# Optimization experiments

Hardware: AMD Instinct MI355X
Metric: run time of the kernel (lower is better)

The kernel has to match this reference:

```python
import jax, jax.numpy as jnp
import numpy as np

B, T, C = 2, 2048, 1024
H = 16
HD = C // H  # 64
SCALE = 0.1 / (HD ** 0.5)


def setup_inputs() -> dict:
    key = jax.random.key(0)
    k1, k2, k3 = jax.random.split(key, 3)
    x = jax.random.normal(k1, (B, T, C), dtype=jnp.float32)
    W_attn = jax.random.normal(k2, (C, 3 * C), dtype=jnp.float32) * (C ** -0.5)
    b_attn = jnp.zeros((3 * C,), dtype=jnp.float32)
    W_proj = jax.random.normal(k3, (C, C), dtype=jnp.float32) * (C ** -0.5)
    b_proj = jnp.zeros((C,), dtype=jnp.float32)
    return {"x": x, "W_attn": W_attn, "b_attn": b_attn, "W_proj": W_proj, "b_proj": b_proj}


def reference(x, W_attn, b_attn, W_proj, b_proj):
    Bx, Tx, Cx = x.shape
    qkv = x @ W_attn + b_attn  # [B,T,3C]
    q, k, v = jnp.split(qkv, 3, axis=-1)
    # [B,T,C] -> [B,H,T,HD]
    q = q.reshape(Bx, Tx, H, HD).transpose(0, 2, 1, 3)
    k = k.reshape(Bx, Tx, H, HD).transpose(0, 2, 1, 3)
    v = v.reshape(Bx, Tx, H, HD).transpose(0, 2, 1, 3)
    # note the extra 0.1 factor baked into this module's scaling
    attn = jnp.einsum('bhqd,bhkd->bhqk', q, k) * SCALE
    causal = jnp.tril(jnp.ones((Tx, Tx), dtype=bool))
    attn = jnp.where(causal[None, None, :, :], attn, -jnp.inf)
    attn = jax.nn.softmax(attn, axis=-1)
    y = jnp.einsum('bhqk,bhkd->bhqd', attn, v)
    y = y.transpose(0, 2, 1, 3).reshape(Bx, Tx, Cx)
    return y @ W_proj + b_proj
```

## Files before the change

kernel.cpp:

```cpp
#include <hip/hip_runtime.h>

typedef unsigned short u16;
typedef unsigned int u32;
typedef float f32x4 __attribute__((ext_vector_type(4)));
typedef float f32x16 __attribute__((ext_vector_type(16)));
typedef __bf16 bf16x8 __attribute__((ext_vector_type(8)));
typedef u16 u16x8 __attribute__((ext_vector_type(8)));
typedef u32 u32x4 __attribute__((ext_vector_type(4)));

#define ATT_SCALE 0.0125f
#define LOG2E 1.4426950408889634f

__device__ __forceinline__ u16 f2bf(float x) {
  unsigned u = __builtin_bit_cast(unsigned, x);
  u += 0x7fffu + ((u >> 16) & 1u);
  return (u16)(u >> 16);
}

__device__ __forceinline__ u32 pack_bf16(float lo, float hi) {
  __bf16 a = (__bf16)lo, b = (__bf16)hi;
  return ((u32)__builtin_bit_cast(u16, b) << 16) | __builtin_bit_cast(u16, a);
}

__device__ __forceinline__ float fexp2(float x) {
  return __builtin_amdgcn_exp2f(x);
}

__device__ __forceinline__ f32x4 mfma16(u16x8 a, u16x8 b, f32x4 c) {
  return __builtin_amdgcn_mfma_f32_16x16x32_bf16(
      __builtin_bit_cast(bf16x8, a), __builtin_bit_cast(bf16x8, b), c, 0, 0, 0);
}

__device__ __forceinline__ f32x16 mfma32(u16x8 a, u16x8 b, f32x16 c) {
  return __builtin_amdgcn_mfma_f32_32x32x16_bf16(
      __builtin_bit_cast(bf16x8, a), __builtin_bit_cast(bf16x8, b), c, 0, 0, 0);
}

__device__ __forceinline__ void gl_lds16(const void* g, void* l) {
  __builtin_amdgcn_global_load_lds(
      (__attribute__((address_space(1))) void*)g,
      (__attribute__((address_space(3))) void*)l, 16, 0, 0);
}

__global__ void k_convert(const float* __restrict__ in, u16* __restrict__ out, int n) {
  int stride = gridDim.x * blockDim.x * 4;
  for (int i = (blockIdx.x * blockDim.x + threadIdx.x) * 4; i < n; i += stride) {
    float4 v = *(const float4*)&in[i];
    ushort4 o;
    o.x = f2bf(v.x); o.y = f2bf(v.y); o.z = f2bf(v.z); o.w = f2bf(v.w);
    *(ushort4*)&out[i] = o;
  }
}

__global__ void k_transpose(const float* __restrict__ in, u16* __restrict__ out,
                            int rows, int cols) {
  __shared__ float tile[32][33];
  int n0 = blockIdx.x * 32;
  int k0 = blockIdx.y * 32;
  int tx = threadIdx.x, ty = threadIdx.y;
#pragma unroll
  for (int i = 0; i < 32; i += 8)
    tile[ty + i][tx] = in[(size_t)(k0 + ty + i) * cols + n0 + tx];
  __syncthreads();
#pragma unroll
  for (int i = 0; i < 32; i += 8)
    out[(size_t)(n0 + ty + i) * rows + k0 + tx] = f2bf(tile[tx][ty + i]);
}

__global__ void k_gemm_qkv(const u16* __restrict__ A, const u16* __restrict__ Bt,
                           const float* __restrict__ bias,
                           u16* __restrict__ qb, u16* __restrict__ kb, u16* __restrict__ vTb) {
  __shared__ u16 Al[128 * 64];
  __shared__ u16 Bl[128 * 64];
  const int tid = threadIdx.x;
  const int lane = tid & 63;
  const int w = tid >> 6;
  const int m0 = blockIdx.y * 128;
  const int n0 = blockIdx.x * 128;
  const int wr = (w >> 1) * 64;
  const int wc = (w & 1) * 64;
  const int lr = lane & 15;
  const int lk = (lane >> 4) * 8;

  f32x4 acc[4][4] = {};

  for (int k0 = 0; k0 < 1024; k0 += 64) {
#pragma unroll
    for (int it = 0; it < 4; ++it) {
      int off = (it * 256 + tid) * 8;
      int r = off >> 6, c = off & 63;
      gl_lds16(&A[(size_t)(m0 + r) * 1024 + k0 + c], &Al[off]);
      gl_lds16(&Bt[(size_t)(n0 + r) * 1024 + k0 + c], &Bl[off]);
    }
    __syncthreads();
#pragma unroll
    for (int kk = 0; kk < 64; kk += 32) {
      u16x8 af[4], bf[4];
#pragma unroll
      for (int i = 0; i < 4; ++i) {
        af[i] = *(const u16x8*)&Al[(wr + i * 16 + lr) * 64 + kk + lk];
        bf[i] = *(const u16x8*)&Bl[(wc + i * 16 + lr) * 64 + kk + lk];
      }
#pragma unroll
      for (int i = 0; i < 4; ++i)
#pragma unroll
        for (int j = 0; j < 4; ++j)
          acc[i][j] = mfma16(af[i], bf[j], acc[i][j]);
    }
    __syncthreads();
  }

#pragma unroll
  for (int i = 0; i < 4; ++i) {
    int rowb = m0 + wr + i * 16 + ((lane >> 4) << 2);
#pragma unroll
    for (int j = 0; j < 4; ++j) {
      int col = n0 + wc + j * 16 + lr;
      float bv = bias[col];
      int which = col >> 10;
      int c = col & 1023;
      int h = c >> 6, d = c & 63;
#pragma unroll
      for (int r = 0; r < 4; ++r) {
        int row = rowb + r;
        int b_ = row >> 11, t = row & 2047;
        int bh = b_ * 16 + h;
        float fv = acc[i][j][r] + bv;
        if (which == 0) {
          qb[((size_t)bh * 2048 + t) * 64 + d] = f2bf(fv * (ATT_SCALE * LOG2E));
        } else if (which == 1) {
          kb[((size_t)bh * 2048 + t) * 64 + d] = f2bf(fv);
        } else {
          vTb[((size_t)bh * 64 + d) * 2048 + t] = f2bf(fv);
        }
      }
    }
  }
}

__device__ __forceinline__ void stage_pair(const u16* __restrict__ kb_bh,
                                           const u16* __restrict__ vT_bh,
                                           u16* Kd, u16* Vd, int kv0, int tid) {
#pragma unroll
  for (int it = 0; it < 4; ++it) {
    int ch = it * 256 + tid;
    int r = ch >> 3, c = ch & 7;
    gl_lds16(&kb_bh[(size_t)(kv0 + r) * 64 + (c ^ (r & 7)) * 8], &Kd[ch * 8]);
    int r2 = ch >> 4, c2 = ch & 15;
    int h2 = c2 >> 3, cc = c2 & 7;
    gl_lds16(&vT_bh[(size_t)r2 * 2048 + kv0 + (h2 * 8 + (cc ^ (r2 & 7))) * 8],
             &Vd[ch * 8]);
  }
}

__global__ __launch_bounds__(256) void k_attn(const u16* __restrict__ qb,
                                              const u16* __restrict__ kb,
                                              const u16* __restrict__ vTb,
                                              u16* __restrict__ yb) {
  __shared__ u16 Kl[2][8192];
  __shared__ u16 Vl[2][8192];

  const int tid = threadIdx.x, lane = tid & 63, w = tid >> 6;
  const int wq = w & 1;
  const int wp = w >> 1;
  const int id = blockIdx.x;
  const int bh = (id & 7) + ((id >> 7) << 3);
  const int pairi = (id >> 3) & 15;
  const int b_ = bh >> 4, h = bh & 15;
  const int ql = lane & 31;
  const int hi = lane >> 5;

  const u16* kb_bh = kb + (size_t)bh * 2048 * 64;
  const u16* vT_bh = vTb + (size_t)bh * 64 * 2048;

#pragma unroll 1
  for (int phase = 0; phase < 2; ++phase) {
    const int qt = phase ? (31 - pairi) : pairi;
    const int q0w = qt * 64 + wq * 32;
    const int qg = q0w + ql;
    const int lim = wq * 32 + ql;

    const u16* qrow = qb + ((size_t)bh * 2048 + qg) * 64;
    u16x8 qf[4];
#pragma unroll
    for (int ks = 0; ks < 4; ++ks)
      qf[ks] = *(const u16x8*)&qrow[ks * 16 + hi * 8];

    f32x16 o0 = {}, o1 = {};
    float mrow = -1e30f, lrow = 0.f;

    const int nkv = qt + 1;
    const int niter = (nkv + 1) >> 1;
    stage_pair(kb_bh, vT_bh, Kl[0], Vl[0], 0, tid);
    __syncthreads();
    int cur = 0;

    for (int it = 0; it < niter; ++it) {
      if (it + 1 < niter)
        stage_pair(kb_bh, vT_bh, Kl[cur ^ 1], Vl[cur ^ 1], (it + 1) * 128, tid);

      const int mytile = 2 * it + wp;
      if (mytile <= qt) {
        const u16* Kc = Kl[cur];
        const u16* Vc = Vl[cur];
        const int rbase = wp * 64;

        f32x16 s0 = {}, s1 = {};
        __builtin_amdgcn_s_setprio(1);
#pragma unroll
        for (int ks = 0; ks < 4; ++ks) {
          int ch = 2 * ks + hi;
          int r0 = rbase + ql, r1 = rbase + 32 + ql;
          u16x8 kf0 = *(const u16x8*)&Kc[r0 * 64 + ((ch ^ (r0 & 7)) * 8)];
          u16x8 kf1 = *(const u16x8*)&Kc[r1 * 64 + ((ch ^ (r1 & 7)) * 8)];
          s0 = mfma32(kf0, qf[ks], s0);
          s1 = mfma32(kf1, qf[ks], s1);
        }
        __builtin_amdgcn_s_setprio(0);

        const bool diag = (mytile == qt);
        float pv[32];
        float tmax = -1e30f;
#pragma unroll
        for (int r = 0; r < 16; ++r) {
          float a = s0[r], b2 = s1[r];
          if (diag) {
            int kl0 = (r & 3) + 8 * (r >> 2) + 4 * hi;
            if (kl0 > lim) a = -1e30f;
            if (kl0 + 32 > lim) b2 = -1e30f;
          }
          pv[r] = a;
          pv[16 + r] = b2;
          tmax = fmaxf(tmax, fmaxf(a, b2));
        }
        float rmax = fmaxf(tmax, __shfl_xor(tmax, 32, 64));

        if (__any(rmax > mrow + 8.0f)) {
          float mn = fmaxf(mrow, rmax);
          float al = fexp2(mrow - mn);
          mrow = mn;
          lrow *= al;
#pragma unroll
          for (int r = 0; r < 16; ++r) { o0[r] *= al; o1[r] *= al; }
        }

        u32 pw[16];
#pragma unroll
        for (int j = 0; j < 16; ++j) {
          float e0 = fexp2(pv[2 * j] - mrow);
          float e1 = fexp2(pv[2 * j + 1] - mrow);
          lrow += e0 + e1;
          pw[j] = pack_bf16(e0, e1);
        }

#pragma unroll
        for (int tt = 0; tt < 2; ++tt)
#pragma unroll
          for (int u = 0; u < 2; ++u)
#pragma unroll
            for (int z = 0; z < 2; ++z) {
              int jA = tt * 8 + u * 4 + z;
              asm volatile("v_permlane32_swap_b32 %0, %1"
                           : "+v"(pw[jA]), "+v"(pw[jA + 2]));
            }

        __builtin_amdgcn_s_setprio(1);
#pragma unroll
        for (int ks = 0; ks < 4; ++ks) {
          u32x4 pwv = {pw[4 * ks], pw[4 * ks + 1], pw[4 * ks + 2], pw[4 * ks + 3]};
          u16x8 pfrag = __builtin_bit_cast(u16x8, pwv);
          int ch = 2 * ks + hi;
          int rv0 = ql, rv1 = 32 + ql;
          u16x8 vf0 = *(const u16x8*)&Vc[rv0 * 128 + (wp * 8 + (ch ^ (rv0 & 7))) * 8];
          u16x8 vf1 = *(const u16x8*)&Vc[rv1 * 128 + (wp * 8 + (ch ^ (rv1 & 7))) * 8];
          o0 = mfma32(vf0, pfrag, o0);
          o1 = mfma32(vf1, pfrag, o1);
        }
        __builtin_amdgcn_s_setprio(0);
      }
      __syncthreads();
      cur ^= 1;
    }

    float* mb = (float*)&Kl[0][0];
    if (wp == 1) {
      float4* dst = (float4*)&mb[(wq * 64 + lane) * 37];
      float4 hd; hd.x = mrow; hd.y = lrow; hd.z = 0.f; hd.w = 0.f;
      dst[0] = hd;
#pragma unroll
      for (int j = 0; j < 4; ++j) {
        float4 t0 = {o0[4 * j], o0[4 * j + 1], o0[4 * j + 2], o0[4 * j + 3]};
        float4 t1 = {o1[4 * j], o1[4 * j + 1], o1[4 * j + 2], o1[4 * j + 3]};
        dst[1 + j] = t0;
        dst[5 + j] = t1;
      }
    }
    __syncthreads();
    if (wp == 0) {
      const float4* src = (const float4*)&mb[(wq * 64 + lane) * 37];
      float4 hd = src[0];
      float m2 = hd.x, l2 = hd.y;
      float m = fmaxf(mrow, m2);
      float a1 = fexp2(mrow - m), a2 = fexp2(m2 - m);
      float l = lrow * a1 + l2 * a2;
      l += __shfl_xor(l, 32, 64);
      float inv = 1.0f / l;

      size_t ybase = ((size_t)b_ * 2048 + qg) * 1024 + h * 64;
#pragma unroll
      for (int dt = 0; dt < 2; ++dt) {
#pragma unroll
        for (int rg = 0; rg < 4; ++rg) {
          float4 po = src[1 + dt * 4 + rg];
          const f32x16& ov = dt ? o1 : o0;
          int d0 = dt * 32 + 8 * rg + 4 * hi;
          ushort4 st;
          st.x = f2bf((ov[rg * 4 + 0] * a1 + po.x * a2) * inv);
          st.y = f2bf((ov[rg * 4 + 1] * a1 + po.y * a2) * inv);
          st.z = f2bf((ov[rg * 4 + 2] * a1 + po.z * a2) * inv);
          st.w = f2bf((ov[rg * 4 + 3] * a1 + po.w * a2) * inv);
          *(ushort4*)&yb[ybase + d0] = st;
        }
      }
    }
    __syncthreads();
  }
}

__global__ void k_gemm_out(const u16* __restrict__ A, const u16* __restrict__ Bt,
                           const float* __restrict__ bias, float* __restrict__ out) {
  __shared__ u16 Al[128 * 64];
  __shared__ u16 Bl[128 * 64];
  const int tid = threadIdx.x;
  const int lane = tid & 63;
  const int w = tid >> 6;
  const int m0 = blockIdx.y * 128;
  const int n0 = blockIdx.x * 128;
  const int wr = (w >> 1) * 64;
  const int wc = (w & 1) * 64;
  const int lr = lane & 15;
  const int lk = (lane >> 4) * 8;

  f32x4 acc[4][4] = {};

  for (int k0 = 0; k0 < 1024; k0 += 64) {
#pragma unroll
    for (int it = 0; it < 4; ++it) {
      int off = (it * 256 + tid) * 8;
      int r = off >> 6, c = off & 63;
      gl_lds16(&A[(size_t)(m0 + r) * 1024 + k0 + c], &Al[off]);
      gl_lds16(&Bt[(size_t)(n0 + r) * 1024 + k0 + c], &Bl[off]);
    }
    __syncthreads();
#pragma unroll
    for (int kk = 0; kk < 64; kk += 32) {
      u16x8 af[4], bf[4];
#pragma unroll
      for (int i = 0; i < 4; ++i) {
        af[i] = *(const u16x8*)&Al[(wr + i * 16 + lr) * 64 + kk + lk];
        bf[i] = *(const u16x8*)&Bl[(wc + i * 16 + lr) * 64 + kk + lk];
      }
#pragma unroll
      for (int i = 0; i < 4; ++i)
#pragma unroll
        for (int j = 0; j < 4; ++j)
          acc[i][j] = mfma16(af[i], bf[j], acc[i][j]);
    }
    __syncthreads();
  }

#pragma unroll
  for (int i = 0; i < 4; ++i) {
    int rowb = m0 + wr + i * 16 + ((lane >> 4) << 2);
#pragma unroll
    for (int j = 0; j < 4; ++j) {
      int col = n0 + wc + j * 16 + lr;
      float bv = bias[col];
#pragma unroll
      for (int r = 0; r < 4; ++r)
        out[(size_t)(rowb + r) * 1024 + col] = acc[i][j][r] + bv;
    }
  }
}

extern "C" void kernel_launch(void* const* d_in, const int* in_sizes, int n_in,
                              void* d_out, int out_size, void* d_ws, size_t ws_size,
                              hipStream_t stream) {
  const float* x      = (const float*)d_in[0];
  const float* W_attn = (const float*)d_in[1];
  const float* b_attn = (const float*)d_in[2];
  const float* W_proj = (const float*)d_in[3];
  const float* b_proj = (const float*)d_in[4];
  float* out = (float*)d_out;

  char* ws = (char*)d_ws;
  const size_t MB = 1024 * 1024;
  u16* x_bf  = (u16*)(ws);
  u16* Wt_a  = (u16*)(ws + 8 * MB);
  u16* Wt_p  = (u16*)(ws + 14 * MB);
  u16* qbf   = (u16*)(ws + 16 * MB);
  u16* kbf   = (u16*)(ws + 24 * MB);
  u16* vTbf  = (u16*)(ws + 32 * MB);
  u16* ybf   = (u16*)(ws + 40 * MB);

  k_convert<<<2048, 256, 0, stream>>>(x, x_bf, 4096 * 1024);
  k_transpose<<<dim3(96, 32), dim3(32, 8), 0, stream>>>(W_attn, Wt_a, 1024, 3072);
  k_transpose<<<dim3(32, 32), dim3(32, 8), 0, stream>>>(W_proj, Wt_p, 1024, 1024);
  k_gemm_qkv<<<dim3(24, 32), 256, 0, stream>>>(x_bf, Wt_a, b_attn, qbf, kbf, vTbf);
  k_attn<<<512, 256, 0, stream>>>(qbf, kbf, vTbf, ybf);
  k_gemm_out<<<dim3(8, 32), 256, 0, stream>>>(ybf, Wt_p, b_proj, out);
}
```

Before: 126.3 us.

## Merge preprocessing kernels, vectorize V-transpose stores, shrink output GEMM tile

Combines the x conversion and both weight transposes into a single launch, which removes two kernel launches and their gaps. The QKV epilogue now writes the transposed V output as packed 4-element stores instead of scattered 2-byte stores. The output projection GEMM moves to 64x128 tiles, doubling the grid to 512 blocks so more CUs are busy, at the cost of less operand reuse per block.

Measured after the change: 112.4 us. -11.0%, faster.

```diff
diff --git a/kernel.cpp b/kernel.cpp
--- a/kernel.cpp
+++ b/kernel.cpp
@@ -42,29 +42,44 @@
       (__attribute__((address_space(3))) void*)l, 16, 0, 0);
 }
 
-__global__ void k_convert(const float* __restrict__ in, u16* __restrict__ out, int n) {
-  int stride = gridDim.x * blockDim.x * 4;
-  for (int i = (blockIdx.x * blockDim.x + threadIdx.x) * 4; i < n; i += stride) {
-    float4 v = *(const float4*)&in[i];
-    ushort4 o;
-    o.x = f2bf(v.x); o.y = f2bf(v.y); o.z = f2bf(v.z); o.w = f2bf(v.w);
-    *(ushort4*)&out[i] = o;
-  }
-}
-
-__global__ void k_transpose(const float* __restrict__ in, u16* __restrict__ out,
-                            int rows, int cols) {
+__global__ void k_pre(const float* __restrict__ x, const float* __restrict__ W_attn,
+                      const float* __restrict__ W_proj, u16* __restrict__ x_bf,
+                      u16* __restrict__ Wt_a, u16* __restrict__ Wt_p) {
   __shared__ float tile[32][33];
-  int n0 = blockIdx.x * 32;
-  int k0 = blockIdx.y * 32;
-  int tx = threadIdx.x, ty = threadIdx.y;
+  const int id = blockIdx.x, tid = threadIdx.x;
+  if (id < 2048) {
+    int base = id * 2048 + tid * 4;
+#pragma unroll
+    for (int s = 0; s < 2; ++s) {
+      int i = base + s * 1024;
+      float4 v = *(const float4*)&x[i];
+      ushort4 o;
+      o.x = f2bf(v.x); o.y = f2bf(v.y); o.z = f2bf(v.z); o.w = f2bf(v.w);
+      *(ushort4*)&x_bf[i] = o;
+    }
+    return;
+  }
+  const float* in;
+  u16* outp;
+  int rows, cols, bx, by;
+  if (id < 5120) {
+    int t2 = id - 2048;
+    bx = t2 % 96; by = t2 / 96;
+    in = W_attn; outp = Wt_a; rows = 1024; cols = 3072;
+  } else {
+    int t3 = id - 5120;
+    bx = t3 & 31; by = t3 >> 5;
+    in = W_proj; outp = Wt_p; rows = 1024; cols = 1024;
+  }
+  int tx = tid & 31, ty = tid >> 5;
+  int n0 = bx * 32, k0 = by * 32;
 #pragma unroll
   for (int i = 0; i < 32; i += 8)
     tile[ty + i][tx] = in[(size_t)(k0 + ty + i) * cols + n0 + tx];
   __syncthreads();
 #pragma unroll
   for (int i = 0; i < 32; i += 8)
-    out[(size_t)(n0 + ty + i) * rows + k0 + tx] = f2bf(tile[tx][ty + i]);
+    outp[(size_t)(n0 + ty + i) * rows + k0 + tx] = f2bf(tile[tx][ty + i]);
 }
 
 __global__ void k_gemm_qkv(const u16* __restrict__ A, const u16* __restrict__ Bt,
@@ -120,18 +135,22 @@
       int which = col >> 10;
       int c = col & 1023;
       int h = c >> 6, d = c & 63;
-#pragma unroll
-      for (int r = 0; r < 4; ++r) {
-        int row = rowb + r;
-        int b_ = row >> 11, t = row & 2047;
-        int bh = b_ * 16 + h;
-        float fv = acc[i][j][r] + bv;
-        if (which == 0) {
-          qb[((size_t)bh * 2048 + t) * 64 + d] = f2bf(fv * (ATT_SCALE * LOG2E));
-        } else if (which == 1) {
-          kb[((size_t)bh * 2048 + t) * 64 + d] = f2bf(fv);
-        } else {
-          vTb[((size_t)bh * 64 + d) * 2048 + t] = f2bf(fv);
+      int b_ = rowb >> 11, t0 = rowb & 2047;
+      int bh = b_ * 16 + h;
+      if (which == 2) {
+        ushort4 st;
+        st.x = f2bf(acc[i][j][0] + bv);
+        st.y = f2bf(acc[i][j][1] + bv);
+        st.z = f2bf(acc[i][j][2] + bv);
+        st.w = f2bf(acc[i][j][3] + bv);
+        *(ushort4*)&vTb[((size_t)bh * 64 + d) * 2048 + t0] = st;
+      } else {
+        u16* dst = (which == 0) ? qb : kb;
+        float sc = (which == 0) ? (ATT_SCALE * LOG2E) : 1.0f;
+#pragma unroll
+        for (int r = 0; r < 4; ++r) {
+          float fv = (acc[i][j][r] + bv) * sc;
+          dst[((size_t)bh * 2048 + t0 + r) * 64 + d] = f2bf(fv);
         }
       }
     }
@@ -329,39 +348,45 @@
 
 __global__ void k_gemm_out(const u16* __restrict__ A, const u16* __restrict__ Bt,
                            const float* __restrict__ bias, float* __restrict__ out) {
-  __shared__ u16 Al[128 * 64];
+  __shared__ u16 Al[64 * 64];
   __shared__ u16 Bl[128 * 64];
   const int tid = threadIdx.x;
   const int lane = tid & 63;
   const int w = tid >> 6;
-  const int m0 = blockIdx.y * 128;
+  const int m0 = blockIdx.y * 64;
   const int n0 = blockIdx.x * 128;
-  const int wr = (w >> 1) * 64;
+  const int wr = (w >> 1) * 32;
   const int wc = (w & 1) * 64;
   const int lr = lane & 15;
   const int lk = (lane >> 4) * 8;
 
-  f32x4 acc[4][4] = {};
+  f32x4 acc[2][4] = {};
 
   for (int k0 = 0; k0 < 1024; k0 += 64) {
 #pragma unroll
+    for (int it = 0; it < 2; ++it) {
+      int ch = it * 256 + tid;
+      int r = ch >> 3, c = (ch & 7) * 8;
+      gl_lds16(&A[(size_t)(m0 + r) * 1024 + k0 + c], &Al[ch * 8]);
+    }
+#pragma unroll
     for (int it = 0; it < 4; ++it) {
-      int off = (it * 256 + tid) * 8;
-      int r = off >> 6, c = off & 63;
-      gl_lds16(&A[(size_t)(m0 + r) * 1024 + k0 + c], &Al[off]);
-      gl_lds16(&Bt[(size_t)(n0 + r) * 1024 + k0 + c], &Bl[off]);
+      int ch = it * 256 + tid;
+      int r = ch >> 3, c = (ch & 7) * 8;
+      gl_lds16(&Bt[(size_t)(n0 + r) * 1024 + k0 + c], &Bl[ch * 8]);
     }
     __syncthreads();
 #pragma unroll
     for (int kk = 0; kk < 64; kk += 32) {
-      u16x8 af[4], bf[4];
-#pragma unroll
-      for (int i = 0; i < 4; ++i) {
+      u16x8 af[2], bf[4];
+#pragma unroll
+      for (int i = 0; i < 2; ++i)
         af[i] = *(const u16x8*)&Al[(wr + i * 16 + lr) * 64 + kk + lk];
-        bf[i] = *(const u16x8*)&Bl[(wc + i * 16 + lr) * 64 + kk + lk];
-      }
-#pragma unroll
-      for (int i = 0; i < 4; ++i)
+#pragma unroll
+      for (int j = 0; j < 4; ++j)
+        bf[j] = *(const u16x8*)&Bl[(wc + j * 16 + lr) * 64 + kk + lk];
+#pragma unroll
+      for (int i = 0; i < 2; ++i)
 #pragma unroll
         for (int j = 0; j < 4; ++j)
           acc[i][j] = mfma16(af[i], bf[j], acc[i][j]);
@@ -370,7 +395,7 @@
   }
 
 #pragma unroll
-  for (int i = 0; i < 4; ++i) {
+  for (int i = 0; i < 2; ++i) {
     int rowb = m0 + wr + i * 16 + ((lane >> 4) << 2);
 #pragma unroll
     for (int j = 0; j < 4; ++j) {
@@ -403,10 +428,8 @@
   u16* vTbf  = (u16*)(ws + 32 * MB);
   u16* ybf   = (u16*)(ws + 40 * MB);
 
-  k_convert<<<2048, 256, 0, stream>>>(x, x_bf, 4096 * 1024);
-  k_transpose<<<dim3(96, 32), dim3(32, 8), 0, stream>>>(W_attn, Wt_a, 1024, 3072);
-  k_transpose<<<dim3(32, 32), dim3(32, 8), 0, stream>>>(W_proj, Wt_p, 1024, 1024);
+  k_pre<<<6144, 256, 0, stream>>>(x, W_attn, W_proj, x_bf, Wt_a, Wt_p);
   k_gemm_qkv<<<dim3(24, 32), 256, 0, stream>>>(x_bf, Wt_a, b_attn, qbf, kbf, vTbf);
   k_attn<<<512, 256, 0, stream>>>(qbf, kbf, vTbf, ybf);
-  k_gemm_out<<<dim3(8, 32), 256, 0, stream>>>(ybf, Wt_p, b_proj, out);
-}
+  k_gemm_out<<<dim3(8, 64), 256, 0, stream>>>(ybf, Wt_p, b_proj, out);
+}
```
